# Performance work log

Measured on AMD Instinct MI355X. Metric: run time of the kernel, lower is better.

Reference implementation:

```python
import jax, jax.numpy as jnp
import numpy as np

N_NODES = 50000
N_EDGES = 800000
NFEAT = 256
NHID = 128
NCLASS = 40
NLAYERS = 3


def setup_inputs() -> dict:
    key = jax.random.key(0)
    ks = jax.random.split(key, 8)
    x = jax.random.normal(ks[0], (N_NODES, NFEAT), dtype=jnp.float32)
    edge_src = jax.random.randint(ks[1], (N_EDGES,), 0, N_NODES, dtype=jnp.int32)
    edge_dst = jax.random.randint(ks[2], (N_EDGES,), 0, N_NODES, dtype=jnp.int32)
    # Kaiming-ish scaled params
    W_in = jax.random.normal(ks[3], (NFEAT, NHID), dtype=jnp.float32) / np.sqrt(NFEAT)
    b_in = jnp.zeros((NHID,), dtype=jnp.float32)
    W_mlps = jax.random.normal(ks[4], (NLAYERS, NHID, NHID), dtype=jnp.float32) / np.sqrt(NHID)
    b_mlps = jnp.zeros((NLAYERS, NHID), dtype=jnp.float32)
    W_out = jax.random.normal(ks[5], (NHID, NCLASS), dtype=jnp.float32) / np.sqrt(NHID)
    b_out = jnp.zeros((NCLASS,), dtype=jnp.float32)
    return {"x": x, "edge_src": edge_src, "edge_dst": edge_dst,
            "W_in": W_in, "b_in": b_in, "W_mlps": W_mlps, "b_mlps": b_mlps,
            "W_out": W_out, "b_out": b_out}


def reference(x, edge_src, edge_dst, W_in, b_in, W_mlps, b_mlps, W_out, b_out):
    # Dropout is identity in eval mode (training=False).
    n = x.shape[0]
    h = jax.nn.relu(x @ W_in + b_in)                       # [N, H]
    for i in range(NLAYERS):
        # GINConv with eps=0: h' = h + sum_{(s->d) in E} h[s] scattered to d
        agg = jax.ops.segment_sum(h[edge_src], edge_dst, num_segments=n)
        h = jax.nn.relu((h + agg) @ W_mlps[i] + b_mlps[i])  # [N, H]
    logits = h @ W_out + b_out                              # [N, C]
    return jax.nn.log_softmax(logits, axis=1)
```

## Files before the change

kernel.cpp:

```cpp
#include <hip/hip_runtime.h>
#include <math.h>

#define NHID 128
#define NFEAT 256
#define NCLASS 40

typedef __bf16 bf16x8 __attribute__((ext_vector_type(8)));
typedef __bf16 bf16x4 __attribute__((ext_vector_type(4)));
typedef float floatx4 __attribute__((ext_vector_type(4)));


__global__ __launch_bounds__(256) void bucket_hist(const int* __restrict__ edst,
                                                   int* __restrict__ bucket_counts,
                                                   int E, int nbuck) {
    __shared__ int lh[256];
    int tid = threadIdx.x;
    lh[tid] = 0;
    __syncthreads();
    int base = blockIdx.x * 4096;
#pragma unroll
    for (int k = 0; k < 16; ++k) {
        int e = base + k * 256 + tid;
        if (e < E) atomicAdd(&lh[edst[e] >> 8], 1);
    }
    __syncthreads();
    if (tid < nbuck && lh[tid]) atomicAdd(&bucket_counts[tid], lh[tid]);
}

__global__ __launch_bounds__(256) void bucket_scan(const int* __restrict__ counts,
                                                   int* __restrict__ start,
                                                   int* __restrict__ cursor,
                                                   int* __restrict__ row_ptr,
                                                   int nbuck, int E, int N) {
    __shared__ int lds[256];
    int tid = threadIdx.x;
    int v = (tid < nbuck) ? counts[tid] : 0;
    lds[tid] = v;
    __syncthreads();
    for (int off = 1; off < 256; off <<= 1) {
        int t = (tid >= off) ? lds[tid - off] : 0;
        __syncthreads();
        lds[tid] += t;
        __syncthreads();
    }
    int excl = lds[tid] - v;
    if (tid < nbuck) { start[tid] = excl; cursor[tid] = excl; }
    if (tid == 0) { start[nbuck] = E; row_ptr[N] = E; }
}

__global__ __launch_bounds__(256) void bucket_scatter(const int* __restrict__ esrc,
                                                      const int* __restrict__ edst,
                                                      int* __restrict__ cursor,
                                                      unsigned int* __restrict__ bdata,
                                                      int E, int nbuck) {
    __shared__ int lh[256];
    __shared__ int lbase[256];
    int tid = threadIdx.x;
    lh[tid] = 0;
    __syncthreads();
    int base = blockIdx.x * 4096;
    unsigned int recs[16];
    short bks[16];
    short lofs[16];
#pragma unroll
    for (int k = 0; k < 16; ++k) {
        int e = base + k * 256 + tid;
        bks[k] = -1;
        if (e < E) {
            int d = edst[e];
            int s = esrc[e];
            int b = d >> 8;
            recs[k] = ((unsigned int)(d & 255) << 16) | (unsigned int)s;
            bks[k] = (short)b;
            lofs[k] = (short)atomicAdd(&lh[b], 1);
        }
    }
    __syncthreads();
    if (tid < nbuck && lh[tid]) lbase[tid] = atomicAdd(&cursor[tid], lh[tid]);
    __syncthreads();
#pragma unroll
    for (int k = 0; k < 16; ++k) {
        if (bks[k] >= 0) bdata[lbase[bks[k]] + lofs[k]] = recs[k];
    }
}

__global__ __launch_bounds__(256) void bucket_finalize(const unsigned int* __restrict__ bdata,
                                                       const int* __restrict__ start,
                                                       int* __restrict__ row_ptr,
                                                       int* __restrict__ srcs,
                                                       int N) {
    __shared__ int hist[256];
    __shared__ int cur[256];
    int b = blockIdx.x;
    int tid = threadIdx.x;
    int s0 = start[b];
    int cnt = start[b + 1] - s0;
    hist[tid] = 0;
    __syncthreads();
    for (int i = tid; i < cnt; i += 256) atomicAdd(&hist[bdata[s0 + i] >> 16], 1);
    __syncthreads();
    int v0 = hist[tid];
    __syncthreads();
    for (int off = 1; off < 256; off <<= 1) {
        int t = (tid >= off) ? hist[tid - off] : 0;
        __syncthreads();
        hist[tid] += t;
        __syncthreads();
    }
    int excl = hist[tid] - v0;
    cur[tid] = excl;
    int node = b * 256 + tid;
    if (node < N) row_ptr[node] = s0 + excl;
    __syncthreads();
    for (int i = tid; i < cnt; i += 256) {
        unsigned int r = bdata[s0 + i];
        int p = atomicAdd(&cur[r >> 16], 1);
        srcs[s0 + p] = (int)(r & 0xffffu);
    }
}

__global__ __launch_bounds__(256) void transpose_split_all(
    const float* __restrict__ Win, const float* __restrict__ Wmlps,
    __bf16* __restrict__ dInHi, __bf16* __restrict__ dInLo,
    __bf16* __restrict__ dMlHi, __bf16* __restrict__ dMlLo) {
    const int TOT_IN = 128 * NFEAT;
    const int TOT_ML = 3 * 128 * NHID;
    int i = blockIdx.x * 256 + threadIdx.x;
    if (i < TOT_IN) {
        int n = i / NFEAT;
        int k = i - n * NFEAT;
        float v = Win[(size_t)k * 128 + n];
        __bf16 h = (__bf16)v;
        dInHi[i] = h;
        dInLo[i] = (__bf16)(v - (float)h);
    } else if (i < TOT_IN + TOT_ML) {
        int r = i - TOT_IN;
        int per = 128 * NHID;
        int l = r / per;
        int rr = r - l * per;
        int n = rr / NHID;
        int k = rr - n * NHID;
        float v = Wmlps[(size_t)l * per + (size_t)k * 128 + n];
        __bf16 h = (__bf16)v;
        dMlHi[r] = h;
        dMlLo[r] = (__bf16)(v - (float)h);
    }
}

__global__ __launch_bounds__(256) void aggregate_fused(const __bf16* __restrict__ hhi,
                                                       const __bf16* __restrict__ hlo,
                                                       const int* __restrict__ row_ptr,
                                                       const int* __restrict__ srcs,
                                                       __bf16* __restrict__ ohi,
                                                       __bf16* __restrict__ olo, int N) {
    int tid = threadIdx.x;
    int node = blockIdx.x * 4 + (tid >> 6);
    if (node >= N) return;
    int lane = tid & 63;
    int g = lane >> 4;
    int c = lane & 15;
    int beg = row_ptr[node];
    int end = row_ptr[node + 1];
    const bf16x8* hv = (const bf16x8*)hhi;

    bf16x8 sh = hv[(size_t)node * 16 + c];
    bf16x8 sl = ((const bf16x8*)hlo)[(size_t)node * 16 + c];

    float a[8], b2[8];
#pragma unroll
    for (int j = 0; j < 8; ++j) { a[j] = 0.f; b2[j] = 0.f; }

    int i = beg;
    for (; i + 16 <= end; i += 16) {
        int s0 = __builtin_nontemporal_load(&srcs[i + g]);
        int s1 = __builtin_nontemporal_load(&srcs[i + 4 + g]);
        int s2 = __builtin_nontemporal_load(&srcs[i + 8 + g]);
        int s3 = __builtin_nontemporal_load(&srcs[i + 12 + g]);
        bf16x8 v0 = hv[(size_t)s0 * 16 + c];
        bf16x8 v1 = hv[(size_t)s1 * 16 + c];
        bf16x8 v2 = hv[(size_t)s2 * 16 + c];
        bf16x8 v3 = hv[(size_t)s3 * 16 + c];
#pragma unroll
        for (int j = 0; j < 8; ++j) {
            a[j] += (float)v0[j] + (float)v2[j];
            b2[j] += (float)v1[j] + (float)v3[j];
        }
    }
    for (; i + 8 <= end; i += 8) {
        int s0 = __builtin_nontemporal_load(&srcs[i + g]);
        int s1 = __builtin_nontemporal_load(&srcs[i + 4 + g]);
        bf16x8 v0 = hv[(size_t)s0 * 16 + c];
        bf16x8 v1 = hv[(size_t)s1 * 16 + c];
#pragma unroll
        for (int j = 0; j < 8; ++j) { a[j] += (float)v0[j]; b2[j] += (float)v1[j]; }
    }
    for (; i < end; i += 4) {
        if (i + g < end) {
            int s = __builtin_nontemporal_load(&srcs[i + g]);
            bf16x8 v = hv[(size_t)s * 16 + c];
#pragma unroll
            for (int j = 0; j < 8; ++j) a[j] += (float)v[j];
        }
    }
#pragma unroll
    for (int j = 0; j < 8; ++j) a[j] += b2[j];
#pragma unroll
    for (int j = 0; j < 8; ++j) a[j] += __shfl_xor(a[j], 16);
#pragma unroll
    for (int j = 0; j < 8; ++j) a[j] += __shfl_xor(a[j], 32);

    if (g == 0) {
        bf16x8 whi, wlo;
#pragma unroll
        for (int j = 0; j < 8; ++j) {
            float v = a[j] + (float)sh[j] + (float)sl[j];
            __bf16 h = (__bf16)v;
            whi[j] = h;
            wlo[j] = (__bf16)(v - (float)h);
        }
        ((bf16x8*)ohi)[(size_t)node * 16 + c] = whi;
        ((bf16x8*)olo)[(size_t)node * 16 + c] = wlo;
    }
}

__global__ __launch_bounds__(256) void gemm_in(
    const float* __restrict__ Af,
    const __bf16* __restrict__ Wthi, const __bf16* __restrict__ Wtlo,
    const float* __restrict__ bias, __bf16* __restrict__ Ohi,
    __bf16* __restrict__ Olo, int M, int K) {
    __shared__ __align__(16) char smem[49152];
    __bf16* sAhi = (__bf16*)smem;
    __bf16* sAlo = (__bf16*)(smem + 8192);
    __bf16* sWhi = (__bf16*)(smem + 16384);
    __bf16* sWlo = (__bf16*)(smem + 32768);

    int tid = threadIdx.x;
    int row0 = blockIdx.x * 64;
    int wave = tid >> 6;
    int l = tid & 63;
    int m16 = l & 15;
    int q = l >> 4;
    int axor = m16 & 7;
    int arow = wave * 16 + m16;

    floatx4 acc[8];
#pragma unroll
    for (int t = 0; t < 8; ++t) acc[t] = (floatx4){0.f, 0.f, 0.f, 0.f};

    for (int k0 = 0; k0 < K; k0 += 64) {
#pragma unroll
        for (int it = 0; it < 2; ++it) {
            int lin = it * 2048 + tid * 8;
            int row = lin >> 6, k = lin & 63;
            int g = min(row0 + row, M - 1);
            int off = row * 64 + (((k >> 3) ^ (row & 7)) << 3);
            float4 v0 = *(const float4*)&Af[(size_t)g * K + k0 + k];
            float4 v1 = *(const float4*)&Af[(size_t)g * K + k0 + k + 4];
            float s[8] = {v0.x, v0.y, v0.z, v0.w, v1.x, v1.y, v1.z, v1.w};
            bf16x8 shi, slo;
#pragma unroll
            for (int j = 0; j < 8; ++j) {
                __bf16 h = (__bf16)s[j];
                shi[j] = h;
                slo[j] = (__bf16)(s[j] - (float)h);
            }
            *(bf16x8*)(sAhi + off) = shi;
            *(bf16x8*)(sAlo + off) = slo;
        }
#pragma unroll
        for (int it = 0; it < 4; ++it) {
            int lin = it * 2048 + tid * 8;
            int n = lin >> 6, kk = lin & 63;
            int off = n * 64 + (((kk >> 3) ^ (n & 7)) << 3);
            *(bf16x8*)(sWhi + off) = *(const bf16x8*)&Wthi[(size_t)n * K + k0 + kk];
            *(bf16x8*)(sWlo + off) = *(const bf16x8*)&Wtlo[(size_t)n * K + k0 + kk];
        }
        __syncthreads();

#pragma unroll
        for (int s = 0; s < 2; ++s) {
            int sw = (((s * 4 + q) ^ axor) << 3);
            bf16x8 ahi = *(bf16x8*)(sAhi + arow * 64 + sw);
            bf16x8 alo = *(bf16x8*)(sAlo + arow * 64 + sw);
#pragma unroll
            for (int t = 0; t < 8; ++t) {
                int n = t * 16 + m16;
                bf16x8 bhi = *(bf16x8*)(sWhi + n * 64 + sw);
                bf16x8 blo = *(bf16x8*)(sWlo + n * 64 + sw);
                acc[t] = __builtin_amdgcn_mfma_f32_16x16x32_bf16(ahi, bhi, acc[t], 0, 0, 0);
                acc[t] = __builtin_amdgcn_mfma_f32_16x16x32_bf16(alo, bhi, acc[t], 0, 0, 0);
                acc[t] = __builtin_amdgcn_mfma_f32_16x16x32_bf16(ahi, blo, acc[t], 0, 0, 0);
            }
        }
        __syncthreads();
    }

    float* eps = (float*)(smem + 16384);
#pragma unroll
    for (int t = 0; t < 8; ++t) {
        int col = t * 16 + m16;
        float bb = bias[col];
#pragma unroll
        for (int i = 0; i < 4; ++i) {
            int row = wave * 16 + q * 4 + i;
            eps[row * 128 + col] = fmaxf(acc[t][i] + bb, 0.f);
        }
    }
    __syncthreads();
#pragma unroll
    for (int it = 0; it < 8; ++it) {
        int lin = it * 1024 + tid * 4;
        int row = lin >> 7, col = lin & 127;
        int g = row0 + row;
        if (g < M) {
            float4 v = *(float4*)(eps + lin);
            bf16x4 hi, lo;
            float vv[4] = {v.x, v.y, v.z, v.w};
#pragma unroll
            for (int j = 0; j < 4; ++j) {
                __bf16 h = (__bf16)vv[j];
                hi[j] = h;
                lo[j] = (__bf16)(vv[j] - (float)h);
            }
            *(bf16x4*)&Ohi[(size_t)g * 128 + col] = hi;
            *(bf16x4*)&Olo[(size_t)g * 128 + col] = lo;
        }
    }
}

__global__ __launch_bounds__(256) void gemm64(
    const __bf16* __restrict__ Ahi, const __bf16* __restrict__ Alo,
    const __bf16* __restrict__ Wthi, const __bf16* __restrict__ Wtlo,
    const float* __restrict__ bias, __bf16* __restrict__ Ohi,
    __bf16* __restrict__ Olo, int M) {
    __shared__ __align__(16) char smem[32768];
    __bf16* sWhi = (__bf16*)smem;
    __bf16* sWlo = (__bf16*)(smem + 16384);

    int tid = threadIdx.x;
    int row0 = (blockIdx.x >> 1) * 64;
    int n0 = (blockIdx.x & 1) * 64;
    int wave = tid >> 6;
    int l = tid & 63;
    int m16 = l & 15;
    int q = l >> 4;
    int garow = min(row0 + wave * 16 + m16, M - 1);

#pragma unroll
    for (int it = 0; it < 4; ++it) {
        int lin = it * 2048 + tid * 8;
        int row = lin >> 7, k = lin & 127;
        int off = row * 128 + (((k >> 3) ^ (row & 7)) << 3);
        *(bf16x8*)(sWhi + off) = *(const bf16x8*)&Wthi[(size_t)(n0 + row) * 128 + k];
        *(bf16x8*)(sWlo + off) = *(const bf16x8*)&Wtlo[(size_t)(n0 + row) * 128 + k];
    }
    __syncthreads();

    floatx4 acc[4];
#pragma unroll
    for (int t = 0; t < 4; ++t) acc[t] = (floatx4){0.f, 0.f, 0.f, 0.f};

#pragma unroll
    for (int fs = 0; fs < 4; ++fs) {
        int kk = fs * 32 + q * 8;
        bf16x8 ahi = *(const bf16x8*)&Ahi[(size_t)garow * 128 + kk];
        bf16x8 alo = *(const bf16x8*)&Alo[(size_t)garow * 128 + kk];
#pragma unroll
        for (int t = 0; t < 4; ++t) {
            int n = t * 16 + m16;
            int soff = n * 128 + (((kk >> 3) ^ (n & 7)) << 3);
            bf16x8 bhi = *(bf16x8*)(sWhi + soff);
            bf16x8 blo = *(bf16x8*)(sWlo + soff);
            acc[t] = __builtin_amdgcn_mfma_f32_16x16x32_bf16(ahi, bhi, acc[t], 0, 0, 0);
            acc[t] = __builtin_amdgcn_mfma_f32_16x16x32_bf16(alo, bhi, acc[t], 0, 0, 0);
            acc[t] = __builtin_amdgcn_mfma_f32_16x16x32_bf16(ahi, blo, acc[t], 0, 0, 0);
        }
    }

    __syncthreads();
    float* eps = (float*)smem;
#pragma unroll
    for (int t = 0; t < 4; ++t) {
        float bb = bias[n0 + t * 16 + m16];
#pragma unroll
        for (int i = 0; i < 4; ++i) {
            int row = wave * 16 + q * 4 + i;
            eps[row * 68 + t * 16 + m16] = fmaxf(acc[t][i] + bb, 0.f);
        }
    }
    __syncthreads();
#pragma unroll
    for (int it = 0; it < 4; ++it) {
        int lin = it * 1024 + tid * 4;
        int row = lin >> 6, col = lin & 63;
        int g = row0 + row;
        if (g < M) {
            float4 v = *(float4*)(eps + row * 68 + col);
            bf16x4 hi, lo;
            float vv[4] = {v.x, v.y, v.z, v.w};
#pragma unroll
            for (int j = 0; j < 4; ++j) {
                __bf16 h = (__bf16)vv[j];
                hi[j] = h;
                lo[j] = (__bf16)(vv[j] - (float)h);
            }
            *(bf16x4*)&Ohi[(size_t)g * 128 + n0 + col] = hi;
            *(bf16x4*)&Olo[(size_t)g * 128 + n0 + col] = lo;
        }
    }
}

__global__ __launch_bounds__(256) void gemm_out(
    const __bf16* __restrict__ Ahi, const __bf16* __restrict__ Alo,
    const __bf16* __restrict__ Wthi, const __bf16* __restrict__ Wtlo,
    const float* __restrict__ bias,
    const float* __restrict__ Wout, const float* __restrict__ bout,
    float* __restrict__ out, int M) {
    __shared__ __align__(16) char smem[57344];
    __bf16* sAhi = (__bf16*)smem;
    __bf16* sAlo = (__bf16*)(smem + 8192);
    __bf16* sWhi = (__bf16*)(smem + 16384);
    __bf16* sWlo = (__bf16*)(smem + 32768);

    int tid = threadIdx.x;
    int row0 = blockIdx.x * 64;
    int wave = tid >> 6;
    int l = tid & 63;
    int m16 = l & 15;
    int q = l >> 4;
    int axor = m16 & 7;
    int arow = wave * 16 + m16;

    floatx4 acc[8];
#pragma unroll
    for (int t = 0; t < 8; ++t) acc[t] = (floatx4){0.f, 0.f, 0.f, 0.f};

    for (int k0 = 0; k0 < 128; k0 += 64) {
#pragma unroll
        for (int it = 0; it < 2; ++it) {
            int lin = it * 2048 + tid * 8;
            int row = lin >> 6, k = lin & 63;
            int g = min(row0 + row, M - 1);
            int off = row * 64 + (((k >> 3) ^ (row & 7)) << 3);
            *(bf16x8*)(sAhi + off) = *(const bf16x8*)&Ahi[(size_t)g * 128 + k0 + k];
            *(bf16x8*)(sAlo + off) = *(const bf16x8*)&Alo[(size_t)g * 128 + k0 + k];
        }
#pragma unroll
        for (int it = 0; it < 4; ++it) {
            int lin = it * 2048 + tid * 8;
            int n = lin >> 6, kk = lin & 63;
            int off = n * 64 + (((kk >> 3) ^ (n & 7)) << 3);
            *(bf16x8*)(sWhi + off) = *(const bf16x8*)&Wthi[(size_t)n * 128 + k0 + kk];
            *(bf16x8*)(sWlo + off) = *(const bf16x8*)&Wtlo[(size_t)n * 128 + k0 + kk];
        }
        __syncthreads();

#pragma unroll
        for (int s = 0; s < 2; ++s) {
            int sw = (((s * 4 + q) ^ axor) << 3);
            bf16x8 ahi = *(bf16x8*)(sAhi + arow * 64 + sw);
            bf16x8 alo = *(bf16x8*)(sAlo + arow * 64 + sw);
#pragma unroll
            for (int t = 0; t < 8; ++t) {
                int n = t * 16 + m16;
                bf16x8 bhi = *(bf16x8*)(sWhi + n * 64 + sw);
                bf16x8 blo = *(bf16x8*)(sWlo + n * 64 + sw);
                acc[t] = __builtin_amdgcn_mfma_f32_16x16x32_bf16(ahi, bhi, acc[t], 0, 0, 0);
                acc[t] = __builtin_amdgcn_mfma_f32_16x16x32_bf16(alo, bhi, acc[t], 0, 0, 0);
                acc[t] = __builtin_amdgcn_mfma_f32_16x16x32_bf16(ahi, blo, acc[t], 0, 0, 0);
            }
        }
        __syncthreads();
    }

    float* eps = (float*)smem;
    float* sWo = (float*)(smem + 34816);
    float* sb  = (float*)(smem + 55296);
#pragma unroll
    for (int t = 0; t < 8; ++t) {
        int col = t * 16 + m16;
        float bb = bias[col];
#pragma unroll
        for (int i = 0; i < 4; ++i) {
            int row = wave * 16 + q * 4 + i;
            eps[row * 132 + col] = fmaxf(acc[t][i] + bb, 0.f);
        }
    }
    for (int i = tid; i < 128 * NCLASS; i += 256) sWo[i] = Wout[i];
    if (tid < NCLASS) sb[tid] = bout[tid];
    __syncthreads();

    int r = tid >> 2;
    int cg = tid & 3;
    float z[10];
#pragma unroll
    for (int j = 0; j < 10; ++j) z[j] = sb[cg * 10 + j];
    for (int k = 0; k < 128; ++k) {
        float a = eps[r * 132 + k];
#pragma unroll
        for (int j = 0; j < 10; ++j) z[j] += a * sWo[k * NCLASS + cg * 10 + j];
    }
    float m = z[0];
#pragma unroll
    for (int j = 1; j < 10; ++j) m = fmaxf(m, z[j]);
    m = fmaxf(m, __shfl_xor(m, 1));
    m = fmaxf(m, __shfl_xor(m, 2));
    float s = 0.f;
#pragma unroll
    for (int j = 0; j < 10; ++j) s += expf(z[j] - m);
    s += __shfl_xor(s, 1);
    s += __shfl_xor(s, 2);
    float lse = m + logf(s);
    int row = row0 + r;
    if (row < M) {
#pragma unroll
        for (int j = 0; j < 10; ++j) out[(size_t)row * NCLASS + cg * 10 + j] = z[j] - lse;
    }
}

extern "C" void kernel_launch(void* const* d_in, const int* in_sizes, int n_in,
                              void* d_out, int out_size, void* d_ws, size_t ws_size,
                              hipStream_t stream) {
    const float* x      = (const float*)d_in[0];
    const int*   esrc   = (const int*)d_in[1];
    const int*   edst   = (const int*)d_in[2];
    const float* W_in   = (const float*)d_in[3];
    const float* b_in   = (const float*)d_in[4];
    const float* W_mlps = (const float*)d_in[5];
    const float* b_mlps = (const float*)d_in[6];
    const float* W_out  = (const float*)d_in[7];
    const float* b_out  = (const float*)d_in[8];
    float* out = (float*)d_out;

    int N = in_sizes[0] / NFEAT;
    int E = in_sizes[1];
    int nbuck = (N + 255) >> 8;

    char* ws = (char*)d_ws;
    size_t hb = (((size_t)N * NHID * sizeof(__bf16)) + 255) & ~(size_t)255;
    __bf16* h_hi_a = (__bf16*)ws;
    __bf16* h_lo_a = (__bf16*)(ws + hb);
    __bf16* h_hi_b = (__bf16*)(ws + 2 * hb);
    __bf16* h_lo_b = (__bf16*)(ws + 3 * hb);
    __bf16* sum_hi = (__bf16*)(ws + 4 * hb);
    __bf16* sum_lo = (__bf16*)(ws + 5 * hb);
    unsigned int* bdata = (unsigned int*)(ws + 4 * hb);
    char* ip = ws + 6 * hb;
    int* row_ptr = (int*)ip;  ip += (((size_t)(N + 1) * 4) + 255) & ~(size_t)255;
    int* srcs    = (int*)ip;  ip += (((size_t)E * 4) + 255) & ~(size_t)255;
    int* bucket_counts = (int*)ip;  ip += 1024;
    int* bucket_start  = (int*)ip;  ip += 1024;
    int* bucket_cursor = (int*)ip;  ip += 1024;
    __bf16* Wt_in_hi   = (__bf16*)ip;  ip += 128 * NFEAT * 2;
    __bf16* Wt_in_lo   = (__bf16*)ip;  ip += 128 * NFEAT * 2;
    __bf16* Wt_mlps_hi = (__bf16*)ip;  ip += 3 * 128 * NHID * 2;
    __bf16* Wt_mlps_lo = (__bf16*)ip;  ip += 3 * 128 * NHID * 2;

    int eb4 = (E + 4095) / 4096;

    hipMemsetAsync(bucket_counts, 0, 1024, stream);
    bucket_hist<<<eb4, 256, 0, stream>>>(edst, bucket_counts, E, nbuck);
    bucket_scan<<<1, 256, 0, stream>>>(bucket_counts, bucket_start, bucket_cursor,
                                       row_ptr, nbuck, E, N);
    bucket_scatter<<<eb4, 256, 0, stream>>>(esrc, edst, bucket_cursor, bdata, E, nbuck);
    bucket_finalize<<<nbuck, 256, 0, stream>>>(bdata, bucket_start, row_ptr, srcs, N);

    transpose_split_all<<<(128 * NFEAT + 3 * 128 * NHID + 255) / 256, 256, 0, stream>>>(
        W_in, W_mlps, Wt_in_hi, Wt_in_lo, Wt_mlps_hi, Wt_mlps_lo);

    int gb = (N + 63) / 64;
    gemm_in<<<gb, 256, 0, stream>>>(x, Wt_in_hi, Wt_in_lo, b_in, h_hi_a, h_lo_a, N, NFEAT);

    __bf16* cur_hi = h_hi_a; __bf16* cur_lo = h_lo_a;
    __bf16* nxt_hi = h_hi_b; __bf16* nxt_lo = h_lo_b;
    for (int i = 0; i < 2; ++i) {
        aggregate_fused<<<(N + 3) / 4, 256, 0, stream>>>(cur_hi, cur_lo, row_ptr, srcs,
                                                         sum_hi, sum_lo, N);
        gemm64<<<gb * 2, 256, 0, stream>>>(
            sum_hi, sum_lo,
            Wt_mlps_hi + (size_t)i * 128 * NHID, Wt_mlps_lo + (size_t)i * 128 * NHID,
            b_mlps + (size_t)i * NHID, nxt_hi, nxt_lo, N);
        __bf16* t;
        t = cur_hi; cur_hi = nxt_hi; nxt_hi = t;
        t = cur_lo; cur_lo = nxt_lo; nxt_lo = t;
    }

    aggregate_fused<<<(N + 3) / 4, 256, 0, stream>>>(cur_hi, cur_lo, row_ptr, srcs,
                                                     sum_hi, sum_lo, N);
    gemm_out<<<gb, 256, 0, stream>>>(sum_hi, sum_lo,
                                     Wt_mlps_hi + (size_t)2 * 128 * NHID,
                                     Wt_mlps_lo + (size_t)2 * 128 * NHID,
                                     b_mlps + (size_t)2 * NHID,
                                     W_out, b_out, out, N);
}
```

Measured before the change: 322.8 us.

## Merge setup kernels into launches and restructure input and output GEMMs to load weights once

The bucket histogram and weight transpose/split are merged into one launch by partitioning blocks, and the CSR finalize is merged with the input GEMM, cutting two kernel launches. The input GEMM is split into two 64-column halves that stage the full transposed weight slice in LDS once and stream A rows straight from global into registers, avoiding per-K-tile A staging and barriers. The output GEMM likewise loads the whole 128x128 weight into LDS up front and reads A fragments directly from global. The changes trade larger LDS use (64KB per block) and lower occupancy, plus uncoalesced direct A loads, for fewer syncs and launches.

```diff
diff --git a/kernel.cpp b/kernel.cpp
--- a/kernel.cpp
+++ b/kernel.cpp
@@ -9,22 +9,50 @@
 typedef __bf16 bf16x4 __attribute__((ext_vector_type(4)));
 typedef float floatx4 __attribute__((ext_vector_type(4)));
 
-
-__global__ __launch_bounds__(256) void bucket_hist(const int* __restrict__ edst,
-                                                   int* __restrict__ bucket_counts,
-                                                   int E, int nbuck) {
+__global__ __launch_bounds__(256) void hist_transpose(
+    const int* __restrict__ edst, int* __restrict__ bucket_counts, int E, int eb4,
+    int nbuck,
+    const float* __restrict__ Win, const float* __restrict__ Wmlps,
+    __bf16* __restrict__ dInHi, __bf16* __restrict__ dInLo,
+    __bf16* __restrict__ dMlHi, __bf16* __restrict__ dMlLo) {
     __shared__ int lh[256];
     int tid = threadIdx.x;
-    lh[tid] = 0;
-    __syncthreads();
-    int base = blockIdx.x * 4096;
-#pragma unroll
-    for (int k = 0; k < 16; ++k) {
-        int e = base + k * 256 + tid;
-        if (e < E) atomicAdd(&lh[edst[e] >> 8], 1);
-    }
-    __syncthreads();
-    if (tid < nbuck && lh[tid]) atomicAdd(&bucket_counts[tid], lh[tid]);
+    int bid = blockIdx.x;
+    if (bid < eb4) {
+        lh[tid] = 0;
+        __syncthreads();
+        int base = bid * 4096;
+#pragma unroll
+        for (int k = 0; k < 16; ++k) {
+            int e = base + k * 256 + tid;
+            if (e < E) atomicAdd(&lh[edst[e] >> 8], 1);
+        }
+        __syncthreads();
+        if (tid < nbuck && lh[tid]) atomicAdd(&bucket_counts[tid], lh[tid]);
+    } else {
+        const int TOT_IN = 128 * NFEAT;
+        const int TOT_ML = 3 * 128 * NHID;
+        int i = (bid - eb4) * 256 + tid;
+        if (i < TOT_IN) {
+            int n = i / NFEAT;
+            int k = i - n * NFEAT;
+            float v = Win[(size_t)k * 128 + n];
+            __bf16 h = (__bf16)v;
+            dInHi[i] = h;
+            dInLo[i] = (__bf16)(v - (float)h);
+        } else if (i < TOT_IN + TOT_ML) {
+            int r = i - TOT_IN;
+            int per = 128 * NHID;
+            int l = r / per;
+            int rr = r - l * per;
+            int n = rr / NHID;
+            int k = rr - n * NHID;
+            float v = Wmlps[(size_t)l * per + (size_t)k * 128 + n];
+            __bf16 h = (__bf16)v;
+            dMlHi[r] = h;
+            dMlLo[r] = (__bf16)(v - (float)h);
+        }
+    }
 }
 
 __global__ __launch_bounds__(256) void bucket_scan(const int* __restrict__ counts,
@@ -84,66 +112,125 @@
     }
 }
 
-__global__ __launch_bounds__(256) void bucket_finalize(const unsigned int* __restrict__ bdata,
-                                                       const int* __restrict__ start,
-                                                       int* __restrict__ row_ptr,
-                                                       int* __restrict__ srcs,
-                                                       int N) {
-    __shared__ int hist[256];
-    __shared__ int cur[256];
-    int b = blockIdx.x;
-    int tid = threadIdx.x;
-    int s0 = start[b];
-    int cnt = start[b + 1] - s0;
-    hist[tid] = 0;
-    __syncthreads();
-    for (int i = tid; i < cnt; i += 256) atomicAdd(&hist[bdata[s0 + i] >> 16], 1);
-    __syncthreads();
-    int v0 = hist[tid];
-    __syncthreads();
-    for (int off = 1; off < 256; off <<= 1) {
-        int t = (tid >= off) ? hist[tid - off] : 0;
-        __syncthreads();
-        hist[tid] += t;
-        __syncthreads();
-    }
-    int excl = hist[tid] - v0;
-    cur[tid] = excl;
-    int node = b * 256 + tid;
-    if (node < N) row_ptr[node] = s0 + excl;
-    __syncthreads();
-    for (int i = tid; i < cnt; i += 256) {
-        unsigned int r = bdata[s0 + i];
-        int p = atomicAdd(&cur[r >> 16], 1);
-        srcs[s0 + p] = (int)(r & 0xffffu);
-    }
-}
-
-__global__ __launch_bounds__(256) void transpose_split_all(
-    const float* __restrict__ Win, const float* __restrict__ Wmlps,
-    __bf16* __restrict__ dInHi, __bf16* __restrict__ dInLo,
-    __bf16* __restrict__ dMlHi, __bf16* __restrict__ dMlLo) {
-    const int TOT_IN = 128 * NFEAT;
-    const int TOT_ML = 3 * 128 * NHID;
-    int i = blockIdx.x * 256 + threadIdx.x;
-    if (i < TOT_IN) {
-        int n = i / NFEAT;
-        int k = i - n * NFEAT;
-        float v = Win[(size_t)k * 128 + n];
-        __bf16 h = (__bf16)v;
-        dInHi[i] = h;
-        dInLo[i] = (__bf16)(v - (float)h);
-    } else if (i < TOT_IN + TOT_ML) {
-        int r = i - TOT_IN;
-        int per = 128 * NHID;
-        int l = r / per;
-        int rr = r - l * per;
-        int n = rr / NHID;
-        int k = rr - n * NHID;
-        float v = Wmlps[(size_t)l * per + (size_t)k * 128 + n];
-        __bf16 h = (__bf16)v;
-        dMlHi[r] = h;
-        dMlLo[r] = (__bf16)(v - (float)h);
+__global__ __launch_bounds__(256) void fin_gemmin64(
+    const unsigned int* __restrict__ bdata, const int* __restrict__ start,
+    int* __restrict__ row_ptr, int* __restrict__ srcs, int N, int nbuck,
+    const float* __restrict__ Af,
+    const __bf16* __restrict__ Wthi, const __bf16* __restrict__ Wtlo,
+    const float* __restrict__ bias, __bf16* __restrict__ Ohi,
+    __bf16* __restrict__ Olo) {
+    __shared__ __align__(16) char smem[65536];
+    int tid = threadIdx.x;
+    if ((int)blockIdx.x < nbuck) {
+        int* hist = (int*)smem;
+        int* cur  = (int*)(smem + 1024);
+        int b = blockIdx.x;
+        int s0 = start[b];
+        int cnt = start[b + 1] - s0;
+        hist[tid] = 0;
+        __syncthreads();
+        for (int i = tid; i < cnt; i += 256) atomicAdd(&hist[bdata[s0 + i] >> 16], 1);
+        __syncthreads();
+        int v0 = hist[tid];
+        __syncthreads();
+        for (int off = 1; off < 256; off <<= 1) {
+            int t = (tid >= off) ? hist[tid - off] : 0;
+            __syncthreads();
+            hist[tid] += t;
+            __syncthreads();
+        }
+        int excl = hist[tid] - v0;
+        cur[tid] = excl;
+        int node = b * 256 + tid;
+        if (node < N) row_ptr[node] = s0 + excl;
+        __syncthreads();
+        for (int i = tid; i < cnt; i += 256) {
+            unsigned int r = bdata[s0 + i];
+            int p = atomicAdd(&cur[r >> 16], 1);
+            srcs[s0 + p] = (int)(r & 0xffffu);
+        }
+        return;
+    }
+    __bf16* sWhi = (__bf16*)smem;
+    __bf16* sWlo = (__bf16*)(smem + 32768);
+    int bix = (int)blockIdx.x - nbuck;
+    int row0 = (bix >> 1) * 64;
+    int n0 = (bix & 1) * 64;
+    int wave = tid >> 6;
+    int l = tid & 63;
+    int m16 = l & 15;
+    int q = l >> 4;
+    int garow = min(row0 + wave * 16 + m16, N - 1);
+
+#pragma unroll
+    for (int it = 0; it < 8; ++it) {
+        int lin = it * 2048 + tid * 8;
+        int wr = lin >> 8, k = lin & 255;
+        int off = wr * 256 + (((k >> 3) ^ (wr & 7)) << 3);
+        *(bf16x8*)(sWhi + off) = *(const bf16x8*)&Wthi[(size_t)(n0 + wr) * 256 + k];
+        *(bf16x8*)(sWlo + off) = *(const bf16x8*)&Wtlo[(size_t)(n0 + wr) * 256 + k];
+    }
+    __syncthreads();
+
+    floatx4 acc[4];
+#pragma unroll
+    for (int t = 0; t < 4; ++t) acc[t] = (floatx4){0.f, 0.f, 0.f, 0.f};
+
+#pragma unroll
+    for (int fs = 0; fs < 8; ++fs) {
+        int kk = fs * 32 + q * 8;
+        float4 v0 = *(const float4*)&Af[(size_t)garow * 256 + kk];
+        float4 v1 = *(const float4*)&Af[(size_t)garow * 256 + kk + 4];
+        float sv[8] = {v0.x, v0.y, v0.z, v0.w, v1.x, v1.y, v1.z, v1.w};
+        bf16x8 ahi, alo;
+#pragma unroll
+        for (int j = 0; j < 8; ++j) {
+            __bf16 h = (__bf16)sv[j];
+            ahi[j] = h;
+            alo[j] = (__bf16)(sv[j] - (float)h);
+        }
+#pragma unroll
+        for (int t = 0; t < 4; ++t) {
+            int n = t * 16 + m16;
+            int soff = n * 256 + (((kk >> 3) ^ (n & 7)) << 3);
+            bf16x8 bhi = *(bf16x8*)(sWhi + soff);
+            bf16x8 blo = *(bf16x8*)(sWlo + soff);
+            acc[t] = __builtin_amdgcn_mfma_f32_16x16x32_bf16(ahi, bhi, acc[t], 0, 0, 0);
+            acc[t] = __builtin_amdgcn_mfma_f32_16x16x32_bf16(alo, bhi, acc[t], 0, 0, 0);
+            acc[t] = __builtin_amdgcn_mfma_f32_16x16x32_bf16(ahi, blo, acc[t], 0, 0, 0);
+        }
+    }
+
+    __syncthreads();
+    float* eps = (float*)smem;
+#pragma unroll
+    for (int t = 0; t < 4; ++t) {
+        float bb = bias[n0 + t * 16 + m16];
+#pragma unroll
+        for (int i = 0; i < 4; ++i) {
+            int row = wave * 16 + q * 4 + i;
+            eps[row * 68 + t * 16 + m16] = fmaxf(acc[t][i] + bb, 0.f);
+        }
+    }
+    __syncthreads();
+#pragma unroll
+    for (int it = 0; it < 4; ++it) {
+        int lin = it * 1024 + tid * 4;
+        int row = lin >> 6, col = lin & 63;
+        int g = row0 + row;
+        if (g < N) {
+            float4 v = *(float4*)(eps + row * 68 + col);
+            bf16x4 hi, lo;
+            float vv[4] = {v.x, v.y, v.z, v.w};
+#pragma unroll
+            for (int j = 0; j < 4; ++j) {
+                __bf16 h = (__bf16)vv[j];
+                hi[j] = h;
+                lo[j] = (__bf16)(vv[j] - (float)h);
+            }
+            *(bf16x4*)&Ohi[(size_t)g * 128 + n0 + col] = hi;
+            *(bf16x4*)&Olo[(size_t)g * 128 + n0 + col] = lo;
+        }
     }
 }
 
@@ -223,111 +310,6 @@
     }
 }
 
-__global__ __launch_bounds__(256) void gemm_in(
-    const float* __restrict__ Af,
-    const __bf16* __restrict__ Wthi, const __bf16* __restrict__ Wtlo,
-    const float* __restrict__ bias, __bf16* __restrict__ Ohi,
-    __bf16* __restrict__ Olo, int M, int K) {
-    __shared__ __align__(16) char smem[49152];
-    __bf16* sAhi = (__bf16*)smem;
-    __bf16* sAlo = (__bf16*)(smem + 8192);
-    __bf16* sWhi = (__bf16*)(smem + 16384);
-    __bf16* sWlo = (__bf16*)(smem + 32768);
-
-    int tid = threadIdx.x;
-    int row0 = blockIdx.x * 64;
-    int wave = tid >> 6;
-    int l = tid & 63;
-    int m16 = l & 15;
-    int q = l >> 4;
-    int axor = m16 & 7;
-    int arow = wave * 16 + m16;
-
-    floatx4 acc[8];
-#pragma unroll
-    for (int t = 0; t < 8; ++t) acc[t] = (floatx4){0.f, 0.f, 0.f, 0.f};
-
-    for (int k0 = 0; k0 < K; k0 += 64) {
-#pragma unroll
-        for (int it = 0; it < 2; ++it) {
-            int lin = it * 2048 + tid * 8;
-            int row = lin >> 6, k = lin & 63;
-            int g = min(row0 + row, M - 1);
-            int off = row * 64 + (((k >> 3) ^ (row & 7)) << 3);
-            float4 v0 = *(const float4*)&Af[(size_t)g * K + k0 + k];
-            float4 v1 = *(const float4*)&Af[(size_t)g * K + k0 + k + 4];
-            float s[8] = {v0.x, v0.y, v0.z, v0.w, v1.x, v1.y, v1.z, v1.w};
-            bf16x8 shi, slo;
-#pragma unroll
-            for (int j = 0; j < 8; ++j) {
-                __bf16 h = (__bf16)s[j];
-                shi[j] = h;
-                slo[j] = (__bf16)(s[j] - (float)h);
-            }
-            *(bf16x8*)(sAhi + off) = shi;
-            *(bf16x8*)(sAlo + off) = slo;
-        }
-#pragma unroll
-        for (int it = 0; it < 4; ++it) {
-            int lin = it * 2048 + tid * 8;
-            int n = lin >> 6, kk = lin & 63;
-            int off = n * 64 + (((kk >> 3) ^ (n & 7)) << 3);
-            *(bf16x8*)(sWhi + off) = *(const bf16x8*)&Wthi[(size_t)n * K + k0 + kk];
-            *(bf16x8*)(sWlo + off) = *(const bf16x8*)&Wtlo[(size_t)n * K + k0 + kk];
-        }
-        __syncthreads();
-
-#pragma unroll
-        for (int s = 0; s < 2; ++s) {
-            int sw = (((s * 4 + q) ^ axor) << 3);
-            bf16x8 ahi = *(bf16x8*)(sAhi + arow * 64 + sw);
-            bf16x8 alo = *(bf16x8*)(sAlo + arow * 64 + sw);
-#pragma unroll
-            for (int t = 0; t < 8; ++t) {
-                int n = t * 16 + m16;
-                bf16x8 bhi = *(bf16x8*)(sWhi + n * 64 + sw);
-                bf16x8 blo = *(bf16x8*)(sWlo + n * 64 + sw);
-                acc[t] = __builtin_amdgcn_mfma_f32_16x16x32_bf16(ahi, bhi, acc[t], 0, 0, 0);
-                acc[t] = __builtin_amdgcn_mfma_f32_16x16x32_bf16(alo, bhi, acc[t], 0, 0, 0);
-                acc[t] = __builtin_amdgcn_mfma_f32_16x16x32_bf16(ahi, blo, acc[t], 0, 0, 0);
-            }
-        }
-        __syncthreads();
-    }
-
-    float* eps = (float*)(smem + 16384);
-#pragma unroll
-    for (int t = 0; t < 8; ++t) {
-        int col = t * 16 + m16;
-        float bb = bias[col];
-#pragma unroll
-        for (int i = 0; i < 4; ++i) {
-            int row = wave * 16 + q * 4 + i;
-            eps[row * 128 + col] = fmaxf(acc[t][i] + bb, 0.f);
-        }
-    }
-    __syncthreads();
-#pragma unroll
-    for (int it = 0; it < 8; ++it) {
-        int lin = it * 1024 + tid * 4;
-        int row = lin >> 7, col = lin & 127;
-        int g = row0 + row;
-        if (g < M) {
-            float4 v = *(float4*)(eps + lin);
-            bf16x4 hi, lo;
-            float vv[4] = {v.x, v.y, v.z, v.w};
-#pragma unroll
-            for (int j = 0; j < 4; ++j) {
-                __bf16 h = (__bf16)vv[j];
-                hi[j] = h;
-                lo[j] = (__bf16)(vv[j] - (float)h);
-            }
-            *(bf16x4*)&Ohi[(size_t)g * 128 + col] = hi;
-            *(bf16x4*)&Olo[(size_t)g * 128 + col] = lo;
-        }
-    }
-}
-
 __global__ __launch_bounds__(256) void gemm64(
     const __bf16* __restrict__ Ahi, const __bf16* __restrict__ Alo,
     const __bf16* __restrict__ Wthi, const __bf16* __restrict__ Wtlo,
@@ -410,16 +392,14 @@
     }
 }
 
-__global__ __launch_bounds__(256) void gemm_out(
+__global__ __launch_bounds__(256) void gemm_out_once(
     const __bf16* __restrict__ Ahi, const __bf16* __restrict__ Alo,
     const __bf16* __restrict__ Wthi, const __bf16* __restrict__ Wtlo,
     const float* __restrict__ bias,
     const float* __restrict__ Wout, const float* __restrict__ bout,
     float* __restrict__ out, int M) {
-    __shared__ __align__(16) char smem[57344];
-    __bf16* sAhi = (__bf16*)smem;
-    __bf16* sAlo = (__bf16*)(smem + 8192);
-    __bf16* sWhi = (__bf16*)(smem + 16384);
+    __shared__ __align__(16) char smem[65536];
+    __bf16* sWhi = (__bf16*)smem;
     __bf16* sWlo = (__bf16*)(smem + 32768);
 
     int tid = threadIdx.x;
@@ -428,51 +408,40 @@
     int l = tid & 63;
     int m16 = l & 15;
     int q = l >> 4;
-    int axor = m16 & 7;
-    int arow = wave * 16 + m16;
+    int garow = min(row0 + wave * 16 + m16, M - 1);
+
+#pragma unroll
+    for (int it = 0; it < 8; ++it) {
+        int lin = it * 2048 + tid * 8;
+        int wr = lin >> 7, k = lin & 127;
+        int off = wr * 128 + (((k >> 3) ^ (wr & 7)) << 3);
+        *(bf16x8*)(sWhi + off) = *(const bf16x8*)&Wthi[(size_t)wr * 128 + k];
+        *(bf16x8*)(sWlo + off) = *(const bf16x8*)&Wtlo[(size_t)wr * 128 + k];
+    }
+    __syncthreads();
 
     floatx4 acc[8];
 #pragma unroll
     for (int t = 0; t < 8; ++t) acc[t] = (floatx4){0.f, 0.f, 0.f, 0.f};
 
-    for (int k0 = 0; k0 < 128; k0 += 64) {
-#pragma unroll
-        for (int it = 0; it < 2; ++it) {
-            int lin = it * 2048 + tid * 8;
-            int row = lin >> 6, k = lin & 63;
-            int g = min(row0 + row, M - 1);
-            int off = row * 64 + (((k >> 3) ^ (row & 7)) << 3);
-            *(bf16x8*)(sAhi + off) = *(const bf16x8*)&Ahi[(size_t)g * 128 + k0 + k];
-            *(bf16x8*)(sAlo + off) = *(const bf16x8*)&Alo[(size_t)g * 128 + k0 + k];
-        }
-#pragma unroll
-        for (int it = 0; it < 4; ++it) {
-            int lin = it * 2048 + tid * 8;
-            int n = lin >> 6, kk = lin & 63;
-            int off = n * 64 + (((kk >> 3) ^ (n & 7)) << 3);
-            *(bf16x8*)(sWhi + off) = *(const bf16x8*)&Wthi[(size_t)n * 128 + k0 + kk];
-            *(bf16x8*)(sWlo + off) = *(const bf16x8*)&Wtlo[(size_t)n * 128 + k0 + kk];
-        }
-        __syncthreads();
-
-#pragma unroll
-        for (int s = 0; s < 2; ++s) {
-            int sw = (((s * 4 + q) ^ axor) << 3);
-            bf16x8 ahi = *(bf16x8*)(sAhi + arow * 64 + sw);
-            bf16x8 alo = *(bf16x8*)(sAlo + arow * 64 + sw);
-#pragma unroll
-            for (int t = 0; t < 8; ++t) {
-                int n = t * 16 + m16;
-                bf16x8 bhi = *(bf16x8*)(sWhi + n * 64 + sw);
-                bf16x8 blo = *(bf16x8*)(sWlo + n * 64 + sw);
-                acc[t] = __builtin_amdgcn_mfma_f32_16x16x32_bf16(ahi, bhi, acc[t], 0, 0, 0);
-                acc[t] = __builtin_amdgcn_mfma_f32_16x16x32_bf16(alo, bhi, acc[t], 0, 0, 0);
-                acc[t] = __builtin_amdgcn_mfma_f32_16x16x32_bf16(ahi, blo, acc[t], 0, 0, 0);
-            }
-        }
-        __syncthreads();
-    }
-
+#pragma unroll
+    for (int fs = 0; fs < 4; ++fs) {
+        int kk = fs * 32 + q * 8;
+        bf16x8 ahi = *(const bf16x8*)&Ahi[(size_t)garow * 128 + kk];
+        bf16x8 alo = *(const bf16x8*)&Alo[(size_t)garow * 128 + kk];
+#pragma unroll
+        for (int t = 0; t < 8; ++t) {
+            int n = t * 16 + m16;
+            int soff = n * 128 + (((kk >> 3) ^ (n & 7)) << 3);
+            bf16x8 bhi = *(bf16x8*)(sWhi + soff);
+            bf16x8 blo = *(bf16x8*)(sWlo + soff);
+            acc[t] = __builtin_amdgcn_mfma_f32_16x16x32_bf16(ahi, bhi, acc[t], 0, 0, 0);
+            acc[t] = __builtin_amdgcn_mfma_f32_16x16x32_bf16(alo, bhi, acc[t], 0, 0, 0);
+            acc[t] = __builtin_amdgcn_mfma_f32_16x16x32_bf16(ahi, blo, acc[t], 0, 0, 0);
+        }
+    }
+
+    __syncthreads();
     float* eps = (float*)smem;
     float* sWo = (float*)(smem + 34816);
     float* sb  = (float*)(smem + 55296);
@@ -557,19 +526,18 @@
     __bf16* Wt_mlps_lo = (__bf16*)ip;  ip += 3 * 128 * NHID * 2;
 
     int eb4 = (E + 4095) / 4096;
+    int gb = (N + 63) / 64;
 
     hipMemsetAsync(bucket_counts, 0, 1024, stream);
-    bucket_hist<<<eb4, 256, 0, stream>>>(edst, bucket_counts, E, nbuck);
+    hist_transpose<<<eb4 + 320, 256, 0, stream>>>(edst, bucket_counts, E, eb4, nbuck,
+                                                  W_in, W_mlps, Wt_in_hi, Wt_in_lo,
+                                                  Wt_mlps_hi, Wt_mlps_lo);
     bucket_scan<<<1, 256, 0, stream>>>(bucket_counts, bucket_start, bucket_cursor,
                                        row_ptr, nbuck, E, N);
     bucket_scatter<<<eb4, 256, 0, stream>>>(esrc, edst, bucket_cursor, bdata, E, nbuck);
-    bucket_finalize<<<nbuck, 256, 0, stream>>>(bdata, bucket_start, row_ptr, srcs, N);
-
-    transpose_split_all<<<(128 * NFEAT + 3 * 128 * NHID + 255) / 256, 256, 0, stream>>>(
-        W_in, W_mlps, Wt_in_hi, Wt_in_lo, Wt_mlps_hi, Wt_mlps_lo);
-
-    int gb = (N + 63) / 64;
-    gemm_in<<<gb, 256, 0, stream>>>(x, Wt_in_hi, Wt_in_lo, b_in, h_hi_a, h_lo_a, N, NFEAT);
+    fin_gemmin64<<<nbuck + gb * 2, 256, 0, stream>>>(bdata, bucket_start, row_ptr, srcs,
+                                                     N, nbuck, x, Wt_in_hi, Wt_in_lo,
+                                                     b_in, h_hi_a, h_lo_a);
 
     __bf16* cur_hi = h_hi_a; __bf16* cur_lo = h_lo_a;
     __bf16* nxt_hi = h_hi_b; __bf16* nxt_lo = h_lo_b;
@@ -587,9 +555,9 @@
 
     aggregate_fused<<<(N + 3) / 4, 256, 0, stream>>>(cur_hi, cur_lo, row_ptr, srcs,
                                                      sum_hi, sum_lo, N);
-    gemm_out<<<gb, 256, 0, stream>>>(sum_hi, sum_lo,
-                                     Wt_mlps_hi + (size_t)2 * 128 * NHID,
-                                     Wt_mlps_lo + (size_t)2 * 128 * NHID,
-                                     b_mlps + (size_t)2 * NHID,
-                                     W_out, b_out, out, N);
-}
+    gemm_out_once<<<gb, 256, 0, stream>>>(sum_hi, sum_lo,
+                                          Wt_mlps_hi + (size_t)2 * 128 * NHID,
+                                          Wt_mlps_lo + (size_t)2 * 128 * NHID,
+                                          b_mlps + (size_t)2 * NHID,
+                                          W_out, b_out, out, N);
+}
```

After: 322.2 us. Within noise of the previous version (-0.2%).
